# Performance work log

Hardware: AMD Instinct MI355X
Metric: run time of the kernel (lower is better)

## Reference

```python
import jax, jax.numpy as jnp
import numpy as np

NUM_NODES = 40000
NUM_EDGES = 400000
DIM = 128
NUM_REL = 502  # num_relation * 2
NUM_HEAD = 1


def setup_inputs() -> dict:
    key = jax.random.key(0)
    ks = jax.random.split(key, 16)
    d = DIM
    return {
        "curr_stat": jax.random.normal(ks[0], (NUM_NODES, d), jnp.float32),
        "last_stat": jax.random.normal(ks[1], (NUM_NODES, d), jnp.float32),
        "relemb_weight": jax.random.normal(ks[2], (NUM_REL, d), jnp.float32),
        "selfrel_weight": jax.random.normal(ks[3], (1, d), jnp.float32),
        "Wq": jax.random.normal(ks[4], (2 * d, d), jnp.float32) * (1.0 / np.sqrt(2 * d)),
        "bq": jax.random.normal(ks[5], (d,), jnp.float32) * 0.02,
        "Wk": jax.random.normal(ks[6], (2 * d, d), jnp.float32) * (1.0 / np.sqrt(2 * d)),
        "bk": jax.random.normal(ks[7], (d,), jnp.float32) * 0.02,
        "Wv": jax.random.normal(ks[8], (d, d), jnp.float32) * (1.0 / np.sqrt(d)),
        "bv": jax.random.normal(ks[9], (d,), jnp.float32) * 0.02,
        "dyn_weight": jax.random.normal(ks[10], (d, d), jnp.float32) * (1.0 / np.sqrt(d)),
        "edge_index": jax.random.randint(ks[11], (2, NUM_EDGES), 0, NUM_NODES, jnp.int32),
        "edge_type": jax.random.randint(ks[12], (NUM_EDGES,), 0, NUM_REL, jnp.int32),
    }


def _segment_softmax(scores, seg, num_segments):
    # scores: [E, H]; softmax over edges sharing the same destination segment
    m = jax.ops.segment_max(scores, seg, num_segments=num_segments)  # [N, H]
    e = jnp.exp(scores - m[seg])
    s = jax.ops.segment_sum(e, seg, num_segments=num_segments)  # [N, H]
    return e / s[seg]


def reference(curr_stat, last_stat, relemb_weight, selfrel_weight,
              Wq, bq, Wk, bk, Wv, bv, dyn_weight,
              edge_index, edge_type):
    N, D = curr_stat.shape
    H = NUM_HEAD
    HD = D // H

    # append self-loop edges for every node, with the dedicated self-relation
    loop = jnp.arange(N, dtype=edge_index.dtype)
    src = jnp.concatenate([edge_index[0], loop])  # [E_total]
    dst = jnp.concatenate([edge_index[1], loop])  # [E_total]
    type_emb = jnp.concatenate(
        [relemb_weight[edge_type], jnp.broadcast_to(selfrel_weight, (N, D))], axis=0)

    E = src.shape[0]
    # linear projections (x @ W + b); torch Linear stores W transposed, same math
    q = (jnp.concatenate([curr_stat[dst], type_emb], -1) @ Wq + bq).reshape(E, H, HD)
    k = (jnp.concatenate([last_stat[src], type_emb], -1) @ Wk + bk).reshape(E, H, HD)
    v = (last_stat[src] @ Wv + bv).reshape(E, H, HD)

    attn = jnp.sum(q * k, axis=-1) / np.sqrt(HD).astype(np.float32)  # [E, H]

    dyn_prob = _segment_softmax(attn, dst, N)   # [E, H]
    sta_prob = _segment_softmax(-attn, dst, N)  # [E, H]

    counts = jax.ops.segment_sum(jnp.ones((E,), jnp.float32), dst, num_segments=N)
    denom = jnp.maximum(counts, 1.0)[:, None]  # scatter-mean denominator

    feat_dyn = jax.ops.segment_sum((dyn_prob[..., None] * v).reshape(E, D), dst,
                                   num_segments=N) / denom
    feat_sta = jax.ops.segment_sum((sta_prob[..., None] * v).reshape(E, D), dst,
                                   num_segments=N) / denom

    # stack (feat_sta, feat_dyn @ dyn_weight) -> [2, N, D]
    return jnp.stack([feat_sta, feat_dyn @ dyn_weight])
```

## Files before the change

### kernel.cpp

```cpp
#include <hip/hip_runtime.h>
#include <hip/hip_bf16.h>
#include <math.h>

#define DIMC 128
#define CS2L (0.08838834764831845f * 1.4426950408889634f)

typedef __attribute__((ext_vector_type(8))) short short8;
typedef __attribute__((ext_vector_type(4))) float floatx4;
typedef __attribute__((ext_vector_type(2))) float f32x2;

static __device__ __forceinline__ unsigned pk2(float lo, float hi) {
    __hip_bfloat162 h = __float22bfloat162_rn(make_float2(lo, hi));
    return *(unsigned*)&h;
}
static __device__ __forceinline__ unsigned short f2bf(float x) {
    union { float f; unsigned int u; } v; v.f = x;
    unsigned int r = v.u + 0x7FFFu + ((v.u >> 16) & 1u);
    return (unsigned short)(r >> 16);
}
static __device__ __forceinline__ f32x2 bfp(unsigned int u) {
    union { unsigned int i; float f; } a, b;
    a.i = u << 16; b.i = u & 0xFFFF0000u;
    f32x2 r; r.x = a.f; r.y = b.f; return r;
}

template<int CTRL>
static __device__ __forceinline__ float dpp_add(float x) {
    int y = __builtin_amdgcn_update_dpp(0, __float_as_int(x), CTRL, 0xF, 0xF, true);
    return x + __int_as_float(y);
}
static __device__ __forceinline__ float red16(float p) {
    p = dpp_add<0xB1>(p);
    p = dpp_add<0x4E>(p);
    p = dpp_add<0x141>(p);
    p = dpp_add<0x140>(p);
    return p;
}

struct PrepArgs {
    const float* W[6];
    unsigned short* F[6];
    float wscale[6];
    const float* relemb; const float* selfrel;
    float* TypeEmb;
    int* deg;
    int R; int N;
};

__global__ __launch_bounds__(64) void prep_all(PrepArgs a)
{
    int b = blockIdx.x;
    int lane = threadIdx.x;
    if (b < 192) {
        int mat = b >> 5, ts = b & 31;
        int s = ts & 3, t = ts >> 2;
        int q = lane >> 4, c = lane & 15;
        const float* W = a.W[mat];
        float sc = a.wscale[mat];
        unsigned short o[8];
        #pragma unroll
        for (int j = 0; j < 8; ++j)
            o[j] = f2bf(W[(long)(s * 32 + q * 8 + j) * DIMC + t * 16 + c] * sc);
        uint4 u;
        u.x = (unsigned)o[0] | ((unsigned)o[1] << 16);
        u.y = (unsigned)o[2] | ((unsigned)o[3] << 16);
        u.z = (unsigned)o[4] | ((unsigned)o[5] << 16);
        u.w = (unsigned)o[6] | ((unsigned)o[7] << 16);
        ((uint4*)a.F[mat])[ts * 64 + lane] = u;
    } else if (b < 192 + a.R + 1) {
        int r = b - 192;
        const float* src = (r < a.R) ? (a.relemb + (long)r * DIMC) : a.selfrel;
        float2 v = ((const float2*)src)[lane];
        ((float2*)(a.TypeEmb + (long)r * DIMC))[lane] = v;
    } else {
        int i = (b - (192 + a.R + 1)) * 64 + lane;
        if (i < a.N) a.deg[i] = 0;
    }
}

struct GemmM5 {
    const float*          Af[5];
    const unsigned short* Ab[5];
    const unsigned short* F[5];
    const float*          bias[5];
    float                 bscale[5];
    float*                outf[5];
    unsigned short*       outb[5];
    int                   ostride[5];
    int                   ooff[5];
    int                   M[5];
    const unsigned short* F2;
    const float*          bias2;
    unsigned short*       outb2;
    const int*            hist_dst;
    int*                  hist_deg;
    int                   hist_E;
};

__global__ __launch_bounds__(256) void gemm_mfma(GemmM5 g)
{
    __shared__ uint4 wlds[2048];

    if (blockIdx.y == 4) {
        int i = blockIdx.x * blockDim.x + threadIdx.x;
        int stride = gridDim.x * blockDim.x;
        for (; i < g.hist_E; i += stride) atomicAdd(&g.hist_deg[g.hist_dst[i]], 1);
        return;
    }

    const int wave = threadIdx.x >> 6;
    const int lane = threadIdx.x & 63;
    const int q = lane >> 4, c = lane & 15;

    if (blockIdx.y == 1) {
        const int M = g.M[1];
        if ((int)blockIdx.x * 64 >= M) return;
        const int rowbase = blockIdx.x * 64 + wave * 16;

        {
            const uint4* Fp = (const uint4*)g.F[1];
            #pragma unroll
            for (int j = 0; j < 8; ++j)
                wlds[threadIdx.x + j * 256] = Fp[threadIdx.x + j * 256];
        }
        int rowA = rowbase + c; if (rowA > M - 1) rowA = M - 1;
        short8 af[4];
        {
            const float* Ar = g.Af[1] + (long)rowA * DIMC + q * 8;
            #pragma unroll
            for (int s = 0; s < 4; ++s) {
                float4 x0 = *(const float4*)(Ar + s * 32);
                float4 x1 = *(const float4*)(Ar + s * 32 + 4);
                uint4 u;
                u.x = pk2(x0.x, x0.y);
                u.y = pk2(x0.z, x0.w);
                u.z = pk2(x1.x, x1.y);
                u.w = pk2(x1.z, x1.w);
                af[s] = *(short8*)&u;
            }
        }
        floatx4 acc[8];
        #pragma unroll
        for (int t = 0; t < 8; ++t) acc[t] = (floatx4){0.f, 0.f, 0.f, 0.f};
        __syncthreads();
        #pragma unroll
        for (int t = 0; t < 8; ++t)
            #pragma unroll
            for (int s = 0; s < 4; ++s) {
                uint4 u = wlds[(t * 4 + s) * 64 + lane];
                acc[t] = __builtin_amdgcn_mfma_f32_16x16x32_bf16(af[s], *(short8*)&u, acc[t], 0, 0, 0);
            }
        __syncthreads();
        {
            const uint4* Fp = (const uint4*)g.F2;
            #pragma unroll
            for (int j = 0; j < 8; ++j)
                wlds[threadIdx.x + j * 256] = Fp[threadIdx.x + j * 256];
        }
        #pragma unroll
        for (int t = 0; t < 8; ++t)
            #pragma unroll
            for (int r = 0; r < 4; ++r) {
                float other = __shfl_xor(acc[t][r], 1);
                int row = rowbase + q * 4 + r;
                if ((lane & 1) == 0 && row < M)
                    ((unsigned*)g.outb[1])[(long)row * 64 + t * 8 + (c >> 1)] = pk2(acc[t][r], other);
            }
        #pragma unroll
        for (int t = 0; t < 8; ++t) {
            float b = g.bias2[t * 16 + c];
            acc[t] = (floatx4){b, b, b, b};
        }
        __syncthreads();
        #pragma unroll
        for (int t = 0; t < 8; ++t)
            #pragma unroll
            for (int s = 0; s < 4; ++s) {
                uint4 u = wlds[(t * 4 + s) * 64 + lane];
                acc[t] = __builtin_amdgcn_mfma_f32_16x16x32_bf16(af[s], *(short8*)&u, acc[t], 0, 0, 0);
            }
        #pragma unroll
        for (int t = 0; t < 8; ++t)
            #pragma unroll
            for (int r = 0; r < 4; ++r) {
                float other = __shfl_xor(acc[t][r], 1);
                int row = rowbase + q * 4 + r;
                if ((lane & 1) == 0 && row < M)
                    ((unsigned*)g.outb2)[(long)row * 64 + t * 8 + (c >> 1)] = pk2(acc[t][r], other);
            }
        return;
    }

    const int which = blockIdx.y;
    const int M = g.M[which];
    if ((int)blockIdx.x * 64 >= M) return;

    const float*          __restrict__ Af   = g.Af[which];
    const unsigned short* __restrict__ Ab   = g.Ab[which];
    const unsigned short* __restrict__ F    = g.F[which];
    const float*          __restrict__ bias = g.bias[which];
    const float bsc = g.bscale[which];
    float*          __restrict__ outf = g.outf[which];
    unsigned short* __restrict__ outb = g.outb[which];
    const int ostride = g.ostride[which];
    const int ooff    = g.ooff[which];
    const int rowbase = blockIdx.x * 64 + wave * 16;

    {
        const uint4* Fp = (const uint4*)F;
        #pragma unroll
        for (int j = 0; j < 8; ++j)
            wlds[threadIdx.x + j * 256] = Fp[threadIdx.x + j * 256];
    }

    int rowA = rowbase + c; if (rowA > M - 1) rowA = M - 1;
    short8 af[4];
    if (Af) {
        const float* Ar = Af + (long)rowA * DIMC + q * 8;
        #pragma unroll
        for (int s = 0; s < 4; ++s) {
            float4 x0 = *(const float4*)(Ar + s * 32);
            float4 x1 = *(const float4*)(Ar + s * 32 + 4);
            uint4 u;
            u.x = pk2(x0.x, x0.y);
            u.y = pk2(x0.z, x0.w);
            u.z = pk2(x1.x, x1.y);
            u.w = pk2(x1.z, x1.w);
            af[s] = *(short8*)&u;
        }
    } else {
        const unsigned short* Ar = Ab + (long)rowA * DIMC + q * 8;
        #pragma unroll
        for (int s = 0; s < 4; ++s) {
            uint4 u = *(const uint4*)(Ar + s * 32);
            af[s] = *(short8*)&u;
        }
    }

    floatx4 acc[8];
    #pragma unroll
    for (int t = 0; t < 8; ++t) {
        float b = bias ? bias[t * 16 + c] * bsc : 0.0f;
        acc[t] = (floatx4){b, b, b, b};
    }

    __syncthreads();

    #pragma unroll
    for (int t = 0; t < 8; ++t)
        #pragma unroll
        for (int s = 0; s < 4; ++s) {
            uint4 u = wlds[(t * 4 + s) * 64 + lane];
            acc[t] = __builtin_amdgcn_mfma_f32_16x16x32_bf16(af[s], *(short8*)&u, acc[t], 0, 0, 0);
        }

    if (outf) {
        #pragma unroll
        for (int t = 0; t < 8; ++t)
            #pragma unroll
            for (int r = 0; r < 4; ++r) {
                int row = rowbase + q * 4 + r;
                if (row < M)
                    outf[(long)row * DIMC + t * 16 + c] = acc[t][r];
            }
    } else {
        #pragma unroll
        for (int t = 0; t < 8; ++t)
            #pragma unroll
            for (int r = 0; r < 4; ++r) {
                float other = __shfl_xor(acc[t][r], 1);
                int row = rowbase + q * 4 + r;
                if ((lane & 1) == 0 && row < M) {
                    unsigned word = pk2(acc[t][r], other);
                    ((unsigned*)outb)[((long)row * 64 + t * 8 + (c >> 1))
                                      * (long)ostride + ooff] = word;
                }
            }
    }
}

__global__ __launch_bounds__(256) void partial_sums(const int* __restrict__ deg,
                                                    int* __restrict__ partial, int N)
{
    __shared__ int sh[256];
    int t = threadIdx.x;
    int beg = blockIdx.x * 1024 + t * 4;
    int s = 0;
    if (beg + 3 < N) { int4 v = *(const int4*)(deg + beg); s = v.x + v.y + v.z + v.w; }
    else { for (int j = 0; j < 4; ++j) if (beg + j < N) s += deg[beg + j]; }
    sh[t] = s;
    __syncthreads();
    for (int d = 128; d >= 1; d >>= 1) {
        if (t < d) sh[t] += sh[t + d];
        __syncthreads();
    }
    if (t == 0) partial[blockIdx.x] = sh[0];
}

__global__ __launch_bounds__(256) void scan_write_offsets(const int* __restrict__ deg,
                                                          const int* __restrict__ partial,
                                                          int* __restrict__ offs,
                                                          int* __restrict__ cursor, int N, int nb)
{
    __shared__ int sh[256];
    __shared__ int sbase;
    int t = threadIdx.x;
    if (t < 64) {
        int v = (t < nb && t < (int)blockIdx.x) ? partial[t] : 0;
        #pragma unroll
        for (int d = 32; d >= 1; d >>= 1) v += __shfl_xor(v, d);
        if (t == 0) sbase = v;
    }
    int beg = blockIdx.x * 1024 + t * 4;
    int d0 = 0, d1 = 0, d2 = 0, d3 = 0;
    if (beg + 3 < N) { int4 v = *(const int4*)(deg + beg); d0 = v.x; d1 = v.y; d2 = v.z; d3 = v.w; }
    else {
        if (beg < N)     d0 = deg[beg];
        if (beg + 1 < N) d1 = deg[beg + 1];
        if (beg + 2 < N) d2 = deg[beg + 2];
        if (beg + 3 < N) d3 = deg[beg + 3];
    }
    int s = d0 + d1 + d2 + d3;
    sh[t] = s;
    __syncthreads();
    for (int d = 1; d < 256; d <<= 1) {
        int v = (t >= d) ? sh[t - d] : 0;
        __syncthreads();
        sh[t] += v;
        __syncthreads();
    }
    int base = sbase + sh[t] - s;
    int o0 = base, o1 = o0 + d0, o2 = o1 + d1, o3 = o2 + d2;
    if (beg < N)     { offs[beg]     = o0; cursor[beg]     = o0; }
    if (beg + 1 < N) { offs[beg + 1] = o1; cursor[beg + 1] = o1; }
    if (beg + 2 < N) { offs[beg + 2] = o2; cursor[beg + 2] = o2; }
    if (beg + 3 < N) { offs[beg + 3] = o3; cursor[beg + 3] = o3; }
}

__global__ void scatter_kernel(const int* __restrict__ src, const int* __restrict__ dst,
                               const int* __restrict__ etype, int* __restrict__ cursor,
                               int2* __restrict__ sedge, int E)
{
    int e = blockIdx.x * blockDim.x + threadIdx.x;
    if (e < E) {
        int d = dst[e];
        int p = atomicAdd(&cursor[d], 1);
        sedge[p] = make_int2(src[e] << 8, etype[e] << 9);
    }
}

__global__ __launch_bounds__(256) void node_kernel(
    const char*  __restrict__ Qb,
    const char*  __restrict__ Kb,
    const char*  __restrict__ Vb,
    const char*  __restrict__ QKb,
    const int* __restrict__ offs, const int* __restrict__ deg,
    const int2* __restrict__ sedge,
    float* __restrict__ out_sta, uint4* __restrict__ feat_dyn,
    int N, int R)
{
    int n = (blockIdx.x * blockDim.x + threadIdx.x) >> 6;
    int lane = threadIdx.x & 63;
    if (n >= N) return;
    const int ql = lane & 15;
    const int qt = lane >> 4;
    const int lo16 = ql << 4;
    const int lo32 = ql << 5;

    int base = offs[n];
    int dcnt = deg[n];
    int etot = dcnt + 1;

    f32x2 qr0, qr1, qr2, qr3;
    {
        uint4 qw = *(const uint4*)(Qb + ((long)n << 8) + lo16);
        qr0 = bfp(qw.x); qr1 = bfp(qw.y); qr2 = bfp(qw.z); qr3 = bfp(qw.w);
    }

    float s_d = 0.0f, s_s = 0.0f;
    f32x2 accd0 = {0.f, 0.f}, accd1 = accd0, accd2 = accd0, accd3 = accd0;
    f32x2 accs0 = accd0, accs1 = accd0, accs2 = accd0, accs3 = accd0;

    const int2 eself = make_int2(n << 8, R << 9);

    int T = (etot + 3) >> 2;
    int2 eCur = eself;
    {
        int i = qt;
        if (i < dcnt) eCur = sedge[base + i];
    }
    for (int it = 0; it < T; ++it) {
        int i = 4 * it + qt;
        bool vv = i < etot;

        int2 eNxt = eself;
        if (it + 1 < T) {
            int inx = 4 * (it + 1) + qt;
            if (inx < dcnt) eNxt = sedge[base + inx];
        }

        uint4 kx  = *(const uint4*)(Kb + eCur.x + lo16);
        uint4 vx  = *(const uint4*)(Vb + eCur.x + lo16);
        uint4 qk0 = *(const uint4*)(QKb + eCur.y + lo32);
        uint4 qk1 = *(const uint4*)(QKb + eCur.y + lo32 + 16);

        f32x2 dp;
        dp  = (qr0 + bfp(qk0.x)) * (bfp(kx.x) + bfp(qk0.y));
        dp += (qr1 + bfp(qk0.z)) * (bfp(kx.y) + bfp(qk0.w));
        dp += (qr2 + bfp(qk1.x)) * (bfp(kx.z) + bfp(qk1.y));
        dp += (qr3 + bfp(qk1.z)) * (bfp(kx.w) + bfp(qk1.w));
        float p = red16(dp.x + dp.y);

        float wd = vv ? exp2f(p)  : 0.0f;
        float ws = vv ? exp2f(-p) : 0.0f;
        s_d += wd; s_s += ws;

        f32x2 v0 = bfp(vx.x), v1 = bfp(vx.y), v2 = bfp(vx.z), v3 = bfp(vx.w);
        accd0 += v0 * wd; accd1 += v1 * wd; accd2 += v2 * wd; accd3 += v3 * wd;
        accs0 += v0 * ws; accs1 += v1 * ws; accs2 += v2 * ws; accs3 += v3 * ws;

        eCur = eNxt;
    }

    #define MRG(x) { x += __shfl_xor(x, 16); x += __shfl_xor(x, 32); }
    MRG(s_d) MRG(s_s)
    MRG(accd0.x) MRG(accd0.y) MRG(accd1.x) MRG(accd1.y)
    MRG(accd2.x) MRG(accd2.y) MRG(accd3.x) MRG(accd3.y)
    MRG(accs0.x) MRG(accs0.y) MRG(accs1.x) MRG(accs1.y)
    MRG(accs2.x) MRG(accs2.y) MRG(accs3.x) MRG(accs3.y)
    #undef MRG

    if (qt == 0) {
        float denom = (float)(dcnt + 1);
        float id_ = 1.0f / (s_d * denom);
        float is_ = 1.0f / (s_s * denom);
        float4* op = (float4*)(out_sta + (long)n * DIMC + ql * 8);
        op[0] = make_float4(accs0.x * is_, accs0.y * is_, accs1.x * is_, accs1.y * is_);
        op[1] = make_float4(accs2.x * is_, accs2.y * is_, accs3.x * is_, accs3.y * is_);
        uint4 w;
        w.x = pk2(accd0.x * id_, accd0.y * id_);
        w.y = pk2(accd1.x * id_, accd1.y * id_);
        w.z = pk2(accd2.x * id_, accd2.y * id_);
        w.w = pk2(accd3.x * id_, accd3.y * id_);
        feat_dyn[(unsigned)n * 16u + ql] = w;
    }
}

extern "C" void kernel_launch(void* const* d_in, const int* in_sizes, int n_in,
                              void* d_out, int out_size, void* d_ws, size_t ws_size,
                              hipStream_t stream)
{
    const float* curr    = (const float*)d_in[0];
    const float* last    = (const float*)d_in[1];
    const float* relemb  = (const float*)d_in[2];
    const float* selfrel = (const float*)d_in[3];
    const float* Wq      = (const float*)d_in[4];
    const float* bq      = (const float*)d_in[5];
    const float* Wk      = (const float*)d_in[6];
    const float* bk      = (const float*)d_in[7];
    const float* Wv      = (const float*)d_in[8];
    const float* bv      = (const float*)d_in[9];
    const float* dynw    = (const float*)d_in[10];
    const int*   eidx    = (const int*)d_in[11];
    const int*   etype   = (const int*)d_in[12];
    float* out = (float*)d_out;

    const int N = in_sizes[0] / DIMC;
    const int E = in_sizes[12];
    const int R = in_sizes[2] / DIMC;
    const int* esrc = eidx;
    const int* edst = eidx + E;

    char* wp = (char*)d_ws;
    auto alloc = [&](size_t bytes) { char* r = wp; wp += (bytes + 15) & ~(size_t)15; return r; };
    size_t nd = (size_t)N * DIMC;
    unsigned short* Qb    = (unsigned short*)alloc((size_t)N * 256);
    unsigned short* Kb    = (unsigned short*)alloc((size_t)N * 256);
    unsigned short* Vb    = (unsigned short*)alloc((size_t)N * 256);
    unsigned short* Fdb   = (unsigned short*)alloc(nd * 2);
    uint4*          QKre  = (uint4*)alloc((size_t)(R + 1) * 32 * 16);
    float*          TypeEmb = (float*)alloc((size_t)(R + 2) * DIMC * 4);
    unsigned short* FW[6];
    for (int m = 0; m < 6; ++m) FW[m] = (unsigned short*)alloc(2048 * 8 * 2);
    int*            deg   = (int*)alloc((size_t)N * 4);
    int*            offs  = (int*)alloc((size_t)N * 4);
    int*            cursor= (int*)alloc((size_t)N * 4);
    int2*           sedge = (int2*)alloc((size_t)E * 8);
    int*            partial = (int*)alloc(256 * 4);

    const int gblk = N / 64;
    const int sblk = (N + 1023) / 1024;

    PrepArgs pa;
    pa.W[0] = Wq;   pa.W[1] = Wk;   pa.W[2] = Wv;
    pa.W[3] = dynw; pa.W[4] = Wq + (size_t)DIMC * DIMC; pa.W[5] = Wk + (size_t)DIMC * DIMC;
    pa.wscale[0] = CS2L; pa.wscale[1] = 1.0f; pa.wscale[2] = 1.0f;
    pa.wscale[3] = 1.0f; pa.wscale[4] = CS2L; pa.wscale[5] = 1.0f;
    for (int m = 0; m < 6; ++m) pa.F[m] = FW[m];
    pa.relemb = relemb; pa.selfrel = selfrel; pa.TypeEmb = TypeEmb;
    pa.deg = deg; pa.R = R; pa.N = N;
    int pgrid = 192 + (R + 1) + (N + 63) / 64;
    hipLaunchKernelGGL(prep_all, dim3(pgrid), dim3(64), 0, stream, pa);

    GemmM5 g5;
    for (int s = 0; s < 5; ++s) { g5.Af[s] = nullptr; g5.Ab[s] = nullptr; g5.outf[s] = nullptr; g5.outb[s] = nullptr; g5.bias[s] = nullptr; g5.bscale[s] = 1.0f; g5.ostride[s] = 1; g5.ooff[s] = 0; g5.M[s] = 0; }
    g5.Af[0] = curr;    g5.F[0] = FW[0]; g5.outb[0] = Qb;  g5.M[0] = N;
    g5.Af[1] = last;    g5.F[1] = FW[1]; g5.outb[1] = Kb;  g5.M[1] = N;
    g5.F2 = FW[2]; g5.bias2 = bv; g5.outb2 = Vb;
    g5.Af[2] = TypeEmb; g5.F[2] = FW[4]; g5.bias[2] = bq;  g5.outb[2] = (unsigned short*)QKre;
    g5.ostride[2] = 2;  g5.ooff[2] = 0;  g5.M[2] = R + 1;  g5.bscale[2] = CS2L;
    g5.Af[3] = TypeEmb; g5.F[3] = FW[5]; g5.bias[3] = bk;  g5.outb[3] = (unsigned short*)QKre;
    g5.ostride[3] = 2;  g5.ooff[3] = 1;  g5.M[3] = R + 1;
    g5.hist_dst = edst; g5.hist_deg = deg; g5.hist_E = E;
    hipLaunchKernelGGL(gemm_mfma, dim3(gblk, 5), dim3(256), 0, stream, g5);

    hipLaunchKernelGGL(partial_sums, dim3(sblk), dim3(256), 0, stream, deg, partial, N);
    hipLaunchKernelGGL(scan_write_offsets, dim3(sblk), dim3(256), 0, stream,
                       deg, partial, offs, cursor, N, sblk);
    hipLaunchKernelGGL(scatter_kernel, dim3((E + 255) / 256), dim3(256), 0, stream,
                       esrc, edst, etype, cursor, sedge, E);

    hipLaunchKernelGGL(node_kernel, dim3((N + 3) / 4), dim3(256), 0, stream,
                       (const char*)Qb, (const char*)Kb, (const char*)Vb, (const char*)QKre,
                       offs, deg, sedge, out, (uint4*)Fdb, N, R);

    GemmM5 gf;
    for (int s = 0; s < 5; ++s) { gf.Af[s] = nullptr; gf.Ab[s] = nullptr; gf.outf[s] = nullptr; gf.outb[s] = nullptr; gf.bias[s] = nullptr; gf.bscale[s] = 1.0f; gf.ostride[s] = 1; gf.ooff[s] = 0; gf.M[s] = 0; }
    gf.Ab[0] = Fdb; gf.F[0] = FW[3]; gf.outf[0] = out + nd; gf.M[0] = N;
    gf.F2 = FW[2]; gf.bias2 = bv; gf.outb2 = Vb;
    gf.hist_dst = edst; gf.hist_deg = deg; gf.hist_E = 0;
    hipLaunchKernelGGL(gemm_mfma, dim3(gblk, 1), dim3(256), 0, stream, gf);
}
```

Baseline: 209.7 us.

## Move degree histogram into prep kernel and overlap edge scatter with GEMMs

The degree histogram now runs inside the prep kernel on dedicated blocks, with deg zeroed by a memset beforehand. The prefix scan is launched before the projection GEMM, and the edge scatter into CSR order is done by the extra blockIdx.y==4 slice of the GEMM launch. This removes the standalone scatter launch and overlaps scatter work with the MFMA projections. The cost is an extra memset launch and a scan that now sits on the critical path ahead of the GEMM.

Result: slower. 219.0 us (+4.4%).

```diff
diff --git a/kernel.cpp b/kernel.cpp
--- a/kernel.cpp
+++ b/kernel.cpp
@@ -4,6 +4,7 @@
 
 #define DIMC 128
 #define CS2L (0.08838834764831845f * 1.4426950408889634f)
+#define HBLK 512
 
 typedef __attribute__((ext_vector_type(8))) short short8;
 typedef __attribute__((ext_vector_type(4))) float floatx4;
@@ -43,7 +44,9 @@
     float wscale[6];
     const float* relemb; const float* selfrel;
     float* TypeEmb;
+    const int* edst;
     int* deg;
+    int E;
     int R; int N;
 };
 
@@ -74,7 +77,8 @@
         ((float2*)(a.TypeEmb + (long)r * DIMC))[lane] = v;
     } else {
         int i = (b - (192 + a.R + 1)) * 64 + lane;
-        if (i < a.N) a.deg[i] = 0;
+        int stride = HBLK * 64;
+        for (; i < a.E; i += stride) atomicAdd(&a.deg[a.edst[i]], 1);
     }
 }
 
@@ -92,9 +96,12 @@
     const unsigned short* F2;
     const float*          bias2;
     unsigned short*       outb2;
-    const int*            hist_dst;
-    int*                  hist_deg;
-    int                   hist_E;
+    const int*            sc_src;
+    const int*            sc_dst;
+    const int*            sc_typ;
+    int*                  sc_cursor;
+    int2*                 sc_sedge;
+    int                   sc_E;
 };
 
 __global__ __launch_bounds__(256) void gemm_mfma(GemmM5 g)
@@ -104,7 +111,11 @@
     if (blockIdx.y == 4) {
         int i = blockIdx.x * blockDim.x + threadIdx.x;
         int stride = gridDim.x * blockDim.x;
-        for (; i < g.hist_E; i += stride) atomicAdd(&g.hist_deg[g.hist_dst[i]], 1);
+        for (; i < g.sc_E; i += stride) {
+            int d = g.sc_dst[i];
+            int p = atomicAdd(&g.sc_cursor[d], 1);
+            g.sc_sedge[p] = make_int2(g.sc_src[i] << 8, g.sc_typ[i] << 9);
+        }
         return;
     }
 
@@ -335,18 +346,6 @@
     if (beg + 1 < N) { offs[beg + 1] = o1; cursor[beg + 1] = o1; }
     if (beg + 2 < N) { offs[beg + 2] = o2; cursor[beg + 2] = o2; }
     if (beg + 3 < N) { offs[beg + 3] = o3; cursor[beg + 3] = o3; }
-}
-
-__global__ void scatter_kernel(const int* __restrict__ src, const int* __restrict__ dst,
-                               const int* __restrict__ etype, int* __restrict__ cursor,
-                               int2* __restrict__ sedge, int E)
-{
-    int e = blockIdx.x * blockDim.x + threadIdx.x;
-    if (e < E) {
-        int d = dst[e];
-        int p = atomicAdd(&cursor[d], 1);
-        sedge[p] = make_int2(src[e] << 8, etype[e] << 9);
-    }
 }
 
 __global__ __launch_bounds__(256) void node_kernel(
@@ -491,6 +490,8 @@
     const int gblk = N / 64;
     const int sblk = (N + 1023) / 1024;
 
+    hipMemsetAsync(deg, 0, (size_t)N * 4, stream);
+
     PrepArgs pa;
     pa.W[0] = Wq;   pa.W[1] = Wk;   pa.W[2] = Wv;
     pa.W[3] = dynw; pa.W[4] = Wq + (size_t)DIMC * DIMC; pa.W[5] = Wk + (size_t)DIMC * DIMC;
@@ -498,9 +499,13 @@
     pa.wscale[3] = 1.0f; pa.wscale[4] = CS2L; pa.wscale[5] = 1.0f;
     for (int m = 0; m < 6; ++m) pa.F[m] = FW[m];
     pa.relemb = relemb; pa.selfrel = selfrel; pa.TypeEmb = TypeEmb;
-    pa.deg = deg; pa.R = R; pa.N = N;
-    int pgrid = 192 + (R + 1) + (N + 63) / 64;
+    pa.edst = edst; pa.deg = deg; pa.E = E; pa.R = R; pa.N = N;
+    int pgrid = 192 + (R + 1) + HBLK;
     hipLaunchKernelGGL(prep_all, dim3(pgrid), dim3(64), 0, stream, pa);
+
+    hipLaunchKernelGGL(partial_sums, dim3(sblk), dim3(256), 0, stream, deg, partial, N);
+    hipLaunchKernelGGL(scan_write_offsets, dim3(sblk), dim3(256), 0, stream,
+                       deg, partial, offs, cursor, N, sblk);
 
     GemmM5 g5;
     for (int s = 0; s < 5; ++s) { g5.Af[s] = nullptr; g5.Ab[s] = nullptr; g5.outf[s] = nullptr; g5.outb[s] = nullptr; g5.bias[s] = nullptr; g5.bscale[s] = 1.0f; g5.ostride[s] = 1; g5.ooff[s] = 0; g5.M[s] = 0; }
@@ -511,14 +516,9 @@
     g5.ostride[2] = 2;  g5.ooff[2] = 0;  g5.M[2] = R + 1;  g5.bscale[2] = CS2L;
     g5.Af[3] = TypeEmb; g5.F[3] = FW[5]; g5.bias[3] = bk;  g5.outb[3] = (unsigned short*)QKre;
     g5.ostride[3] = 2;  g5.ooff[3] = 1;  g5.M[3] = R + 1;
-    g5.hist_dst = edst; g5.hist_deg = deg; g5.hist_E = E;
+    g5.sc_src = esrc; g5.sc_dst = edst; g5.sc_typ = etype;
+    g5.sc_cursor = cursor; g5.sc_sedge = sedge; g5.sc_E = E;
     hipLaunchKernelGGL(gemm_mfma, dim3(gblk, 5), dim3(256), 0, stream, g5);
-
-    hipLaunchKernelGGL(partial_sums, dim3(sblk), dim3(256), 0, stream, deg, partial, N);
-    hipLaunchKernelGGL(scan_write_offsets, dim3(sblk), dim3(256), 0, stream,
-                       deg, partial, offs, cursor, N, sblk);
-    hipLaunchKernelGGL(scatter_kernel, dim3((E + 255) / 256), dim3(256), 0, stream,
-                       esrc, edst, etype, cursor, sedge, E);
 
     hipLaunchKernelGGL(node_kernel, dim3((N + 3) / 4), dim3(256), 0, stream,
                        (const char*)Qb, (const char*)Kb, (const char*)Vb, (const char*)QKre,
@@ -528,6 +528,7 @@
     for (int s = 0; s < 5; ++s) { gf.Af[s] = nullptr; gf.Ab[s] = nullptr; gf.outf[s] = nullptr; gf.outb[s] = nullptr; gf.bias[s] = nullptr; gf.bscale[s] = 1.0f; gf.ostride[s] = 1; gf.ooff[s] = 0; gf.M[s] = 0; }
     gf.Ab[0] = Fdb; gf.F[0] = FW[3]; gf.outf[0] = out + nd; gf.M[0] = N;
     gf.F2 = FW[2]; gf.bias2 = bv; gf.outb2 = Vb;
-    gf.hist_dst = edst; gf.hist_deg = deg; gf.hist_E = 0;
+    gf.sc_src = esrc; gf.sc_dst = edst; gf.sc_typ = etype;
+    gf.sc_cursor = cursor; gf.sc_sedge = sedge; gf.sc_E = 0;
     hipLaunchKernelGGL(gemm_mfma, dim3(gblk, 1), dim3(256), 0, stream, gf);
 }
```
